# Kernel optimization log

Hardware: AMD Instinct MI355X
Metric: run time of the kernel (lower is better)

The kernel has to match this reference:

```python
import jax, jax.numpy as jnp
import numpy as np

N_LAYER, N_HEAD, D_MODEL, D_K, D_HIDDEN = 8, 8, 512, 64, 2048
N_CONTEXT, N_DICT, MAG = 1024, 8192, 0.05
B, T = 8, 1024


def _sinusoidal_pos(n_context, d_model):
    i2 = np.arange(0, d_model, 2)
    inv = 1.0 / (10000.0 ** (i2 / d_model))
    ang = np.arange(n_context, dtype=np.float32)[:, None] * inv[None, :]
    pe = np.zeros((1, n_context, d_model), np.float32)
    pe[0, :, 0::2] = np.sin(ang)
    pe[0, :, 1::2] = np.cos(ang)
    return jnp.asarray(pe)


def setup_inputs() -> dict:
    key = jax.random.key(0)
    ks = jax.random.split(key, 10)
    p = lambda k, *s: jax.random.normal(k, s, jnp.float32) * MAG
    return {
        "x": jax.random.randint(ks[0], (B, T), 0, N_DICT),
        "last_only": False,
        "capture_stats": False,
        "embedding": p(ks[1], N_DICT, D_MODEL),
        "pos_embedding": _sinusoidal_pos(N_CONTEXT, D_MODEL),  # fixedpos='True', not trained
        "wq": p(ks[2], N_LAYER, N_HEAD, D_MODEL, D_K),
        "wk": p(ks[3], N_LAYER, N_HEAD, D_MODEL, D_K),
        "wv": p(ks[4], N_LAYER, N_HEAD, D_MODEL, D_MODEL),
        "mlp0": p(ks[5], N_LAYER, D_MODEL, D_HIDDEN),
        "mlpb": p(ks[6], N_LAYER, 1, D_HIDDEN),
        "mlp1": p(ks[7], N_LAYER, D_HIDDEN, D_MODEL),
        "unembedding": p(ks[8], D_MODEL, N_DICT),
        "bias": p(ks[9], 1, 1, N_DICT),
    }


def _ln(x):
    # torch LayerNorm(elementwise_affine=False, bias=False), eps=1e-5, biased var
    mu = jnp.mean(x, axis=-1, keepdims=True)
    var = jnp.mean((x - mu) ** 2, axis=-1, keepdims=True)
    return (x - mu) * jax.lax.rsqrt(var + 1e-5)


def reference(x, last_only, capture_stats, embedding, pos_embedding,
              wq, wk, wv, mlp0, mlpb, mlp1, unembedding, bias):
    del capture_stats  # stats path disabled (capture_stats=False)
    t = x.shape[1]
    h = embedding[x] + pos_embedding[:, :t, :]   # [B,T,M]
    h = _ln(h)                                    # enorm='True', lmul = 1/ldiv = 1
    mask = jnp.tril(jnp.ones((t, t), dtype=bool))

    def layer(h, params):
        wq_l, wk_l, wv_l, m0, mb, m1 = params
        q = jnp.einsum('btm,hmq->bhtq', h, wq_l)
        k = jnp.einsum('bom,hmk->bhok', h, wk_l)
        v = jnp.einsum('bom,hmv->bhov', h, wv_l)
        attn = jnp.einsum('bhtq,bhoq->bhto', q, k)
        # exp(clamp(.,max=50)) then tril then sum-normalize (NOT softmax)
        attn = jnp.where(mask, jnp.exp(jnp.minimum(attn, 50.0)), 0.0)
        attn = attn / (jnp.sum(attn, axis=-1, keepdims=True) + 1e-10)
        vsum = jnp.einsum('bhto,bhov->btv', attn, v)  # sums over heads
        h = _ln(h + vsum)                              # amul = 1, lmul = 1
        y = jax.nn.relu(jnp.einsum('btm,mh->bth', h, m0) + mb)
        y = jnp.einsum('bth,hm->btm', y, m1)
        h = _ln(h + y)                                 # pmul = 1, lmul = 1
        return h, None

    h, _ = jax.lax.scan(layer, h, (wq, wk, wv, mlp0, mlpb, mlp1))
    if last_only:
        h = h[:, -1:, :]
    return jnp.einsum('btm,md->btd', h, unembedding) + bias
```

## Files before the change

### kernel.cpp

```cpp
#include <hip/hip_runtime.h>
#include <hip/hip_bf16.h>

#define BB 8
#define TT 1024
#define DM 512
#define NH 8
#define DK 64
#define DH 2048
#define NL 8
#define ND 8192

typedef __attribute__((ext_vector_type(8))) short short8v;
typedef __attribute__((ext_vector_type(8))) _Float16 f16x8;
typedef __attribute__((ext_vector_type(4))) float f32x4;
typedef __attribute__((ext_vector_type(4))) unsigned short ushort4v;
typedef unsigned short u16;

#define MFMA16(a, b, c) __builtin_amdgcn_mfma_f32_16x16x32_bf16(a, b, c, 0, 0, 0)
#define MFMAH(a, b, c)  __builtin_amdgcn_mfma_f32_16x16x32_f16(a, b, c, 0, 0, 0)

__device__ __forceinline__ u16 bf16_bits(float f) {
  union { __hip_bfloat16 h; u16 u; } cv;
  cv.h = __float2bfloat16(f);
  return cv.u;
}
__device__ __forceinline__ float bits_to_f32(u16 u) {
  union { __hip_bfloat16 h; u16 u; } cv;
  cv.u = u;
  return __bfloat162float(cv.h);
}

__device__ __forceinline__ void gload16(const void* g, void* l) {
  __builtin_amdgcn_global_load_lds(
      (const __attribute__((address_space(1))) unsigned int*)g,
      (__attribute__((address_space(3))) unsigned int*)l, 16, 0, 0);
}

#define WAITVM(N) asm volatile("s_waitcnt vmcnt(" #N ")" ::: "memory")
#define BAR() { __builtin_amdgcn_s_barrier(); asm volatile("" ::: "memory"); }

__device__ __forceinline__ void block_reduce2(float& a, float& b) {
  #pragma unroll
  for (int off = 32; off > 0; off >>= 1) {
    a += __shfl_down(a, off, 64);
    b += __shfl_down(b, off, 64);
  }
  __shared__ float sa[4], sb[4];
  int w = threadIdx.x >> 6;
  if ((threadIdx.x & 63) == 0) { sa[w] = a; sb[w] = b; }
  __syncthreads();
  if (threadIdx.x == 0) {
    sa[0] = sa[0] + sa[1] + sa[2] + sa[3];
    sb[0] = sb[0] + sb[1] + sb[2] + sb[3];
  }
  __syncthreads();
  a = sa[0]; b = sb[0];
}

__global__ __launch_bounds__(256) void embed_ln_kernel(
    const int* __restrict__ x, const float* __restrict__ emb,
    const float* __restrict__ pos, float* __restrict__ h,
    u16* __restrict__ hh, _Float16* __restrict__ hf) {
  int bt = blockIdx.x;
  int t = bt & (TT - 1);
  int tid = threadIdx.x;
  int row = x[bt];
  float v0 = emb[(size_t)row * DM + tid]       + pos[(size_t)t * DM + tid];
  float v1 = emb[(size_t)row * DM + tid + 256] + pos[(size_t)t * DM + tid + 256];
  float s = v0 + v1, sq = v0 * v0 + v1 * v1;
  block_reduce2(s, sq);
  float mu  = s * (1.0f / DM);
  float var = sq * (1.0f / DM) - mu * mu;
  float rs  = rsqrtf(var + 1e-5f);
  float r0 = (v0 - mu) * rs, r1 = (v1 - mu) * rs;
  h[(size_t)bt * DM + tid] = r0;
  h[(size_t)bt * DM + tid + 256] = r1;
  hh[(size_t)bt * DM + tid] = bf16_bits(r0);
  hh[(size_t)bt * DM + tid + 256] = bf16_bits(r1);
  hf[(size_t)bt * DM + tid] = (_Float16)r0;
  hf[(size_t)bt * DM + tid + 256] = (_Float16)r1;
}

template<bool BF16ADD>
__global__ __launch_bounds__(256) void ln_residual_kernel(
    float* __restrict__ h, const void* __restrict__ add_, int rowStride, int nsum,
    u16* __restrict__ hh, _Float16* __restrict__ hf) {
  int bt = blockIdx.x;
  int tid = threadIdx.x;
  size_t base = (size_t)bt * (size_t)rowStride;
  float v0 = h[(size_t)bt * DM + tid];
  float v1 = h[(size_t)bt * DM + tid + 256];
  if (BF16ADD) {
    const u16* add = (const u16*)add_;
    for (int i = 0; i < nsum; ++i) {
      v0 += bits_to_f32(add[base + (size_t)i * DM + tid]);
      v1 += bits_to_f32(add[base + (size_t)i * DM + tid + 256]);
    }
  } else {
    const float* add = (const float*)add_;
    for (int i = 0; i < nsum; ++i) {
      v0 += add[base + (size_t)i * DM + tid];
      v1 += add[base + (size_t)i * DM + tid + 256];
    }
  }
  float s = v0 + v1, sq = v0 * v0 + v1 * v1;
  block_reduce2(s, sq);
  float mu  = s * (1.0f / DM);
  float var = sq * (1.0f / DM) - mu * mu;
  float rs  = rsqrtf(var + 1e-5f);
  float r0 = (v0 - mu) * rs, r1 = (v1 - mu) * rs;
  h[(size_t)bt * DM + tid] = r0;
  h[(size_t)bt * DM + tid + 256] = r1;
  hh[(size_t)bt * DM + tid] = bf16_bits(r0);
  hh[(size_t)bt * DM + tid + 256] = bf16_bits(r1);
  hf[(size_t)bt * DM + tid] = (_Float16)r0;
  hf[(size_t)bt * DM + tid + 256] = (_Float16)r1;
}

__global__ __launch_bounds__(256) void transpose_layer(
    const float* __restrict__ wq, const float* __restrict__ wk,
    const float* __restrict__ wv, const float* __restrict__ w0,
    const float* __restrict__ w1,
    _Float16* __restrict__ qT, _Float16* __restrict__ kT,
    u16* __restrict__ vT, u16* __restrict__ t0, u16* __restrict__ t1) {
  __shared__ float T[64][65];
  int t = blockIdx.x;
  const float* in;
  _Float16* of = nullptr;
  u16* ob = nullptr;
  int K, Nb;
  if (t < 64)       { in = wq; of = qT; K = 512;  Nb = 64; }
  else if (t < 128) { in = wk; of = kT; K = 512;  Nb = 64;   t -= 64; }
  else if (t < 640) { in = wv; ob = vT; K = 512;  Nb = 512;  t -= 128; }
  else if (t < 896) { in = w0; ob = t0; K = 512;  Nb = 2048; t -= 640; }
  else              { in = w1; ob = t1; K = 2048; Nb = 512;  t -= 896; }
  int ntx = K >> 6;
  int k0 = (t % ntx) * 64, n0 = (t / ntx) * 64;
  int g = n0 / Nb;
  const float* src = in + (size_t)g * K * Nb + (n0 - g * Nb);
  int tid = threadIdx.x;
  #pragma unroll
  for (int rep = 0; rep < 16; ++rep) {
    int idx = rep * 256 + tid;
    int i = idx >> 6, j = idx & 63;
    T[i][j] = src[(size_t)(k0 + i) * Nb + j];
  }
  __syncthreads();
  #pragma unroll
  for (int rep = 0; rep < 16; ++rep) {
    int idx = rep * 256 + tid;
    int j = idx >> 6, i = idx & 63;
    float v = T[i][j];
    size_t oa = (size_t)(n0 + j) * K + k0 + i;
    if (of) of[oa] = (_Float16)v;
    else    ob[oa] = bf16_bits(v);
  }
}

__global__ __launch_bounds__(256) void transpose_ue(
    const float* __restrict__ ue, u16* __restrict__ ueT) {
  __shared__ float T[64][65];
  int tid = threadIdx.x;
  int k0 = blockIdx.x * 64, n0 = blockIdx.y * 64;
  #pragma unroll
  for (int rep = 0; rep < 16; ++rep) {
    int idx = rep * 256 + tid;
    int i = idx >> 6, j = idx & 63;
    T[i][j] = ue[(size_t)(k0 + i) * ND + n0 + j];
  }
  __syncthreads();
  #pragma unroll
  for (int rep = 0; rep < 16; ++rep) {
    int idx = rep * 256 + tid;
    int j = idx >> 6, i = idx & 63;
    ueT[(size_t)(n0 + j) * DM + k0 + i] = bf16_bits(T[i][j]);
  }
}

template<int MODE>
__global__ __launch_bounds__(256, 2) void gemm_mfma(
    const u16* __restrict__ A, const u16* __restrict__ Bt,
    const float* __restrict__ bias, void* __restrict__ Oo,
    int M, int N, int K) {
  __shared__ u16 As[2][8192];
  __shared__ u16 Bs[2][8192];
  int tid = threadIdx.x;
  int lane = tid & 63, w = tid >> 6;
  int l15 = lane & 15, g = lane >> 4;
  int m0 = blockIdx.x * 128, n0 = blockIdx.y * 128;
  int wr = w >> 1, wc = w & 1;
  int nt = K >> 6;

  f32x4 acc[4][4];
  #pragma unroll
  for (int i = 0; i < 4; ++i)
    #pragma unroll
    for (int j = 0; j < 4; ++j)
      #pragma unroll
      for (int r = 0; r < 4; ++r) acc[i][j][r] = 0.f;

  auto stage = [&](int t, int buf) {
    int k0 = t << 6;
    #pragma unroll
    for (int j = 0; j < 4; ++j) {
      int idx = j * 256 + tid;
      int row = idx >> 3, cs = (idx & 7) ^ (row & 7);
      gload16(A + (size_t)(m0 + row) * K + k0 + cs * 8, &As[buf][idx * 8]);
    }
    #pragma unroll
    for (int j = 0; j < 4; ++j) {
      int idx = j * 256 + tid;
      int row = idx >> 3, cs = (idx & 7) ^ (row & 7);
      gload16(Bt + (size_t)(n0 + row) * K + k0 + cs * 8, &Bs[buf][idx * 8]);
    }
  };

  stage(0, 0);
  for (int t = 0; t < nt; ++t) {
    int cur = t & 1;
    if (t + 1 < nt) {
      stage(t + 1, cur ^ 1);
      WAITVM(8);
    } else {
      WAITVM(0);
    }
    BAR();
    short8v af[4][2], bf[4][2];
    #pragma unroll
    for (int mi = 0; mi < 4; ++mi) {
      int row = wr * 64 + mi * 16 + l15;
      #pragma unroll
      for (int ks = 0; ks < 2; ++ks) {
        int ch = (ks * 4 + g) ^ (row & 7);
        af[mi][ks] = *(const short8v*)&As[cur][row * 64 + ch * 8];
      }
    }
    #pragma unroll
    for (int ni = 0; ni < 4; ++ni) {
      int row = wc * 64 + ni * 16 + l15;
      #pragma unroll
      for (int ks = 0; ks < 2; ++ks) {
        int ch = (ks * 4 + g) ^ (row & 7);
        bf[ni][ks] = *(const short8v*)&Bs[cur][row * 64 + ch * 8];
      }
    }
    __builtin_amdgcn_s_setprio(1);
    #pragma unroll
    for (int mi = 0; mi < 4; ++mi)
      #pragma unroll
      for (int ni = 0; ni < 4; ++ni) {
        acc[mi][ni] = MFMA16(af[mi][0], bf[ni][0], acc[mi][ni]);
        acc[mi][ni] = MFMA16(af[mi][1], bf[ni][1], acc[mi][ni]);
      }
    __builtin_amdgcn_s_setprio(0);
    BAR();
  }

  #pragma unroll
  for (int mi = 0; mi < 4; ++mi) {
    #pragma unroll
    for (int ni = 0; ni < 4; ++ni) {
      int mrow = m0 + wr * 64 + mi * 16 + g * 4;
      int ncol = n0 + wc * 64 + ni * 16 + l15;
      if (MODE == 0) {
        int head = ncol >> 9, dv = ncol & (DM - 1);
        int bb = mrow >> 10, t0 = mrow & (TT - 1);
        ushort4v pk;
        #pragma unroll
        for (int r = 0; r < 4; ++r) pk[r] = bf16_bits(acc[mi][ni][r]);
        *(ushort4v*)((u16*)Oo + ((((size_t)bb * NH + head) * DM + dv) << 10) + t0) = pk;
      } else if (MODE == 1) {
        float bv = bias[ncol];
        #pragma unroll
        for (int r = 0; r < 4; ++r)
          ((u16*)Oo)[(size_t)(mrow + r) * N + ncol] =
              bf16_bits(fmaxf(acc[mi][ni][r] + bv, 0.f));
      } else if (MODE == 2) {
        #pragma unroll
        for (int r = 0; r < 4; ++r)
          ((float*)Oo)[(size_t)(mrow + r) * N + ncol] = acc[mi][ni][r];
      } else {
        float bv = bias[ncol];
        #pragma unroll
        for (int r = 0; r < 4; ++r)
          ((float*)Oo)[(size_t)(mrow + r) * N + ncol] = acc[mi][ni][r] + bv;
      }
    }
  }
}

__global__ __launch_bounds__(256, 2) void gemm_qk_f16(
    const _Float16* __restrict__ A, const _Float16* __restrict__ Bt,
    _Float16* __restrict__ Oq, int K) {
  __shared__ _Float16 As[2][8192];
  __shared__ _Float16 Bs[2][8192];
  int tid = threadIdx.x;
  int lane = tid & 63, w = tid >> 6;
  int l15 = lane & 15, g = lane >> 4;
  int m0 = blockIdx.x * 128, n0 = blockIdx.y * 128;
  int wr = w >> 1, wc = w & 1;
  int nt = K >> 6;

  f32x4 acc[4][4];
  #pragma unroll
  for (int i = 0; i < 4; ++i)
    #pragma unroll
    for (int j = 0; j < 4; ++j)
      #pragma unroll
      for (int r = 0; r < 4; ++r) acc[i][j][r] = 0.f;

  auto stage = [&](int t, int buf) {
    int k0 = t << 6;
    #pragma unroll
    for (int j = 0; j < 4; ++j) {
      int idx = j * 256 + tid;
      int row = idx >> 3, cs = (idx & 7) ^ (row & 7);
      gload16(A + (size_t)(m0 + row) * K + k0 + cs * 8, &As[buf][idx * 8]);
    }
    #pragma unroll
    for (int j = 0; j < 4; ++j) {
      int idx = j * 256 + tid;
      int row = idx >> 3, cs = (idx & 7) ^ (row & 7);
      gload16(Bt + (size_t)(n0 + row) * K + k0 + cs * 8, &Bs[buf][idx * 8]);
    }
  };

  stage(0, 0);
  for (int t = 0; t < nt; ++t) {
    int cur = t & 1;
    if (t + 1 < nt) {
      stage(t + 1, cur ^ 1);
      WAITVM(8);
    } else {
      WAITVM(0);
    }
    BAR();
    f16x8 af[4][2], bf[4][2];
    #pragma unroll
    for (int mi = 0; mi < 4; ++mi) {
      int row = wr * 64 + mi * 16 + l15;
      #pragma unroll
      for (int ks = 0; ks < 2; ++ks) {
        int ch = (ks * 4 + g) ^ (row & 7);
        af[mi][ks] = *(const f16x8*)&As[cur][row * 64 + ch * 8];
      }
    }
    #pragma unroll
    for (int ni = 0; ni < 4; ++ni) {
      int row = wc * 64 + ni * 16 + l15;
      #pragma unroll
      for (int ks = 0; ks < 2; ++ks) {
        int ch = (ks * 4 + g) ^ (row & 7);
        bf[ni][ks] = *(const f16x8*)&Bs[cur][row * 64 + ch * 8];
      }
    }
    __builtin_amdgcn_s_setprio(1);
    #pragma unroll
    for (int mi = 0; mi < 4; ++mi)
      #pragma unroll
      for (int ni = 0; ni < 4; ++ni) {
        acc[mi][ni] = MFMAH(af[mi][0], bf[ni][0], acc[mi][ni]);
        acc[mi][ni] = MFMAH(af[mi][1], bf[ni][1], acc[mi][ni]);
      }
    __builtin_amdgcn_s_setprio(0);
    BAR();
  }

  #pragma unroll
  for (int mi = 0; mi < 4; ++mi) {
    #pragma unroll
    for (int ni = 0; ni < 4; ++ni) {
      int mrow = m0 + wr * 64 + mi * 16 + g * 4;
      int ncol = n0 + wc * 64 + ni * 16 + l15;
      int head = ncol >> 6, dk = ncol & (DK - 1);
      int bb = mrow >> 10;
      #pragma unroll
      for (int r = 0; r < 4; ++r) {
        int t = (mrow + r) & (TT - 1);
        Oq[(((size_t)bb * NH + head) * TT + t) * DK + dk] = (_Float16)acc[mi][ni][r];
      }
    }
  }
}

__global__ __launch_bounds__(256, 2) void attn_mfma_kernel(
    const _Float16* __restrict__ qp, const _Float16* __restrict__ kp,
    const __hip_bfloat16* __restrict__ vt_, u16* __restrict__ o) {
  __shared__ __align__(16) u16 Pl[2][64 * 64];
  __shared__ __align__(16) _Float16 Kl[2][64 * 64];
  __shared__ float rs_lds[64];

  const u16* vtp = (const u16*)vt_;
  int tid = threadIdx.x;
  int lane = tid & 63;
  int w = tid >> 6;
  int l15 = lane & 15, g = lane >> 4;
  int blk = blockIdx.x;
  int bh = blk & 63;
  int tt = 15 - (blk >> 6);

  if (tid < 64) rs_lds[tid] = 0.f;

  auto stageK = [&](int ot, int buf) {
    int ob = ot * 64;
    #pragma unroll
    for (int j = 0; j < 2; ++j) {
      int idx = j * 256 + tid;
      int row = idx >> 3, cs = (idx & 7) ^ (row & 7);
      gload16(kp + ((size_t)bh * TT + ob + row) * DK + cs * 8, &Kl[buf][idx * 8]);
    }
  };

  size_t qbase = (((size_t)bh * TT) + tt * 64 + w * 16 + l15) * DK + g * 8;
  f16x8 qf[2];
  qf[0] = *(const f16x8*)(qp + qbase);
  qf[1] = *(const f16x8*)(qp + qbase + 32);

  f32x4 oacc[4][8];
  #pragma unroll
  for (int qt = 0; qt < 4; ++qt)
    #pragma unroll
    for (int dv = 0; dv < 8; ++dv)
      #pragma unroll
      for (int r = 0; r < 4; ++r) oacc[qt][dv][r] = 0.f;

  stageK(0, 0);
  WAITVM(0);
  __syncthreads();

  for (int ot = 0; ot <= tt; ++ot) {
    int ob = ot * 64;
    bool diag = (ot == tt);
    int buf = ot & 1;
    if (ot < tt) stageK(ot + 1, buf ^ 1);
    f32x4 sacc[4];
    #pragma unroll
    for (int ct = 0; ct < 4; ++ct)
      #pragma unroll
      for (int r = 0; r < 4; ++r) sacc[ct][r] = 0.f;
    __builtin_amdgcn_s_setprio(1);
    #pragma unroll
    for (int ct = 0; ct < 4; ++ct) {
      int row = ct * 16 + l15;
      f16x8 k0 = *(const f16x8*)&Kl[buf][row * 64 + ((g) ^ (row & 7)) * 8];
      f16x8 k1 = *(const f16x8*)&Kl[buf][row * 64 + ((4 + g) ^ (row & 7)) * 8];
      sacc[ct] = MFMAH(qf[0], k0, sacc[ct]);
      sacc[ct] = MFMAH(qf[1], k1, sacc[ct]);
    }
    __builtin_amdgcn_s_setprio(0);
    size_t vbase = ((size_t)bh * DM + w * 128 + l15) * TT + ob + g * 8;
    short8v vf0[8];
    #pragma unroll
    for (int dv = 0; dv < 8; ++dv)
      vf0[dv] = *(const short8v*)(vtp + vbase + (size_t)dv * 16 * TT);
    float psum[4] = {0.f, 0.f, 0.f, 0.f};
    #pragma unroll
    for (int ct = 0; ct < 4; ++ct) {
      #pragma unroll
      for (int r = 0; r < 4; ++r) {
        float s = sacc[ct][r];
        float p = __expf(fminf(s, 50.f));
        if (diag && (ct * 16 + l15 > w * 16 + g * 4 + r)) p = 0.f;
        psum[r] += p;
        int q = w * 16 + g * 4 + r;
        int byte = (q * 128 + (ct * 16 + l15) * 2) ^ ((q & 7) << 4);
        *(u16*)((char*)Pl[buf] + byte) = bf16_bits(p);
      }
    }
    #pragma unroll
    for (int r = 0; r < 4; ++r) {
      float v = psum[r];
      v += __shfl_xor(v, 1, 16);
      v += __shfl_xor(v, 2, 16);
      v += __shfl_xor(v, 4, 16);
      v += __shfl_xor(v, 8, 16);
      if (l15 == 0) rs_lds[w * 16 + g * 4 + r] += v;
    }
    WAITVM(0);
    BAR();
    short8v vf1[8];
    #pragma unroll
    for (int dv = 0; dv < 8; ++dv)
      vf1[dv] = *(const short8v*)(vtp + vbase + 32 + (size_t)dv * 16 * TT);
    short8v pf[4];
    #pragma unroll
    for (int qt = 0; qt < 4; ++qt) {
      int q = qt * 16 + l15;
      int byte = (q * 128 + g * 16) ^ ((q & 7) << 4);
      pf[qt] = *(short8v*)((char*)Pl[buf] + byte);
    }
    __builtin_amdgcn_s_setprio(1);
    #pragma unroll
    for (int dv = 0; dv < 8; ++dv)
      #pragma unroll
      for (int qt = 0; qt < 4; ++qt)
        oacc[qt][dv] = MFMA16(pf[qt], vf0[dv], oacc[qt][dv]);
    __builtin_amdgcn_s_setprio(0);
    #pragma unroll
    for (int qt = 0; qt < 4; ++qt) {
      int q = qt * 16 + l15;
      int byte = (q * 128 + 64 + g * 16) ^ ((q & 7) << 4);
      pf[qt] = *(short8v*)((char*)Pl[buf] + byte);
    }
    __builtin_amdgcn_s_setprio(1);
    #pragma unroll
    for (int dv = 0; dv < 8; ++dv)
      #pragma unroll
      for (int qt = 0; qt < 4; ++qt)
        oacc[qt][dv] = MFMA16(pf[qt], vf1[dv], oacc[qt][dv]);
    __builtin_amdgcn_s_setprio(0);
  }
  __syncthreads();
  int b = bh >> 3, hh2 = bh & 7;
  #pragma unroll
  for (int qt = 0; qt < 4; ++qt) {
    #pragma unroll
    for (int r = 0; r < 4; ++r) {
      int q = qt * 16 + g * 4 + r;
      float rs = 1.0f / (rs_lds[q] + 1e-10f);
      size_t rowbase = ((size_t)(b * TT + tt * 64 + q)) * (NH * DM) + hh2 * DM + w * 128 + l15;
      #pragma unroll
      for (int dv = 0; dv < 8; ++dv)
        o[rowbase + dv * 16] = bf16_bits(oacc[qt][dv][r] * rs);
    }
  }
}

extern "C" void kernel_launch(void* const* d_in, const int* in_sizes, int n_in,
                              void* d_out, int out_size, void* d_ws, size_t ws_size,
                              hipStream_t stream) {
  (void)in_sizes; (void)n_in; (void)out_size; (void)ws_size;
  const int*   x   = (const int*)d_in[0];
  const float* emb = (const float*)d_in[3];
  const float* pos = (const float*)d_in[4];
  const float* wq  = (const float*)d_in[5];
  const float* wk  = (const float*)d_in[6];
  const float* wv  = (const float*)d_in[7];
  const float* m0  = (const float*)d_in[8];
  const float* mb  = (const float*)d_in[9];
  const float* m1  = (const float*)d_in[10];
  const float* ue  = (const float*)d_in[11];
  const float* ub  = (const float*)d_in[12];
  float* out = (float*)d_out;
  float* ws  = (float*)d_ws;

  const int M = BB * TT;

  float*    h    = ws;
  u16*      hh   = (u16*)(ws + 4194304);
  _Float16* hf16 = (_Float16*)(ws + 6291456);
  float*    yb   = ws + 8388608;
  u16*      ueT  = (u16*)(ws + 12582912);

  u16* outus = (u16*)d_out;
  u16* vt = outus;
  _Float16* qf16 = (_Float16*)(outus + 33554432);
  _Float16* kf16 = (_Float16*)(outus + 37748736);
  u16* wT = outus + 41943040;
  _Float16* wqT = (_Float16*)wT;
  _Float16* wkT = (_Float16*)(wT + 262144);
  u16* wvT = wT + 524288;
  u16* w0T = wT + 2621440;
  u16* w1T = wT + 3670016;
  u16* Ob  = outus + 67108864;
  u16* hid = outus;

  embed_ln_kernel<<<M, 256, 0, stream>>>(x, emb, pos, h, hh, hf16);

  for (int l = 0; l < NL; ++l) {
    transpose_layer<<<1152, 256, 0, stream>>>(
        wq + (size_t)l * NH * DM * DK, wk + (size_t)l * NH * DM * DK,
        wv + (size_t)l * NH * DM * DM, m0 + (size_t)l * DM * DH,
        m1 + (size_t)l * DH * DM,
        wqT, wkT, wvT, w0T, w1T);
    gemm_qk_f16<<<dim3(64, 4), 256, 0, stream>>>(hf16, wqT, qf16, DM);
    gemm_qk_f16<<<dim3(64, 4), 256, 0, stream>>>(hf16, wkT, kf16, DM);
    gemm_mfma<0><<<dim3(64, 32), 256, 0, stream>>>(hh, wvT, nullptr, vt, M, NH * DM, DM);
    attn_mfma_kernel<<<BB * NH * (TT / 64), 256, 0, stream>>>(
        qf16, kf16, (const __hip_bfloat16*)vt, Ob);
    ln_residual_kernel<true><<<M, 256, 0, stream>>>(h, Ob, NH * DM, NH, hh, hf16);
    gemm_mfma<1><<<dim3(64, 16), 256, 0, stream>>>(hh, w0T, mb + (size_t)l * DH, hid, M, DH, DM);
    gemm_mfma<2><<<dim3(64, 4), 256, 0, stream>>>(hid, w1T, nullptr, yb, M, DM, DH);
    ln_residual_kernel<false><<<M, 256, 0, stream>>>(h, yb, DM, 1, hh, hf16);
  }
  transpose_ue<<<dim3(8, 128), 256, 0, stream>>>(ue, ueT);
  gemm_mfma<3><<<dim3(64, 64), 256, 0, stream>>>(hh, ueT, ub, out, M, ND, DM);
}
```

Baseline: 2.351 ms.

## Reassociate attention-value product to apply Wv after attention over hidden states

Computes attn·h per head (using a transposed bf16 copy of h) and then multiplies the concatenated head outputs by a stacked Wv (K=4096) in one GEMM. This replaces the large V projection producing 8 heads × 512 dims and the 8-way head summation in the residual LN. The Q and K projections are also merged into a single launch. It adds a per-layer transpose of h and reorders the rounding points, since the attention now runs on bf16 h instead of a bf16 V.

```diff
diff --git a/kernel.cpp b/kernel.cpp
--- a/kernel.cpp
+++ b/kernel.cpp
@@ -83,25 +83,20 @@
 
 template<bool BF16ADD>
 __global__ __launch_bounds__(256) void ln_residual_kernel(
-    float* __restrict__ h, const void* __restrict__ add_, int rowStride, int nsum,
+    float* __restrict__ h, const void* __restrict__ add_,
     u16* __restrict__ hh, _Float16* __restrict__ hf) {
   int bt = blockIdx.x;
   int tid = threadIdx.x;
-  size_t base = (size_t)bt * (size_t)rowStride;
   float v0 = h[(size_t)bt * DM + tid];
   float v1 = h[(size_t)bt * DM + tid + 256];
   if (BF16ADD) {
     const u16* add = (const u16*)add_;
-    for (int i = 0; i < nsum; ++i) {
-      v0 += bits_to_f32(add[base + (size_t)i * DM + tid]);
-      v1 += bits_to_f32(add[base + (size_t)i * DM + tid + 256]);
-    }
+    v0 += bits_to_f32(add[(size_t)bt * DM + tid]);
+    v1 += bits_to_f32(add[(size_t)bt * DM + tid + 256]);
   } else {
     const float* add = (const float*)add_;
-    for (int i = 0; i < nsum; ++i) {
-      v0 += add[base + (size_t)i * DM + tid];
-      v1 += add[base + (size_t)i * DM + tid + 256];
-    }
+    v0 += add[(size_t)bt * DM + tid];
+    v1 += add[(size_t)bt * DM + tid + 256];
   }
   float s = v0 + v1, sq = v0 * v0 + v1 * v1;
   block_reduce2(s, sq);
@@ -117,23 +112,45 @@
   hf[(size_t)bt * DM + tid + 256] = (_Float16)r1;
 }
 
+__global__ __launch_bounds__(256) void transpose_hT(
+    const float* __restrict__ h, u16* __restrict__ hT) {
+  __shared__ float T[64][65];
+  int t0 = blockIdx.x * 64;
+  int d0 = blockIdx.y * 64;
+  int tid = threadIdx.x;
+  #pragma unroll
+  for (int rep = 0; rep < 16; ++rep) {
+    int idx = rep * 256 + tid;
+    int i = idx >> 6, j = idx & 63;
+    T[i][j] = h[(size_t)(t0 + i) * DM + d0 + j];
+  }
+  __syncthreads();
+  #pragma unroll
+  for (int rep = 0; rep < 16; ++rep) {
+    int idx = rep * 256 + tid;
+    int j = idx >> 6, i = idx & 63;
+    hT[(size_t)(d0 + j) * (BB * TT) + t0 + i] = bf16_bits(T[i][j]);
+  }
+}
+
 __global__ __launch_bounds__(256) void transpose_layer(
     const float* __restrict__ wq, const float* __restrict__ wk,
     const float* __restrict__ wv, const float* __restrict__ w0,
     const float* __restrict__ w1,
-    _Float16* __restrict__ qT, _Float16* __restrict__ kT,
-    u16* __restrict__ vT, u16* __restrict__ t0, u16* __restrict__ t1) {
+    _Float16* __restrict__ qkT, u16* __restrict__ vT2,
+    u16* __restrict__ t0o, u16* __restrict__ t1o) {
   __shared__ float T[64][65];
   int t = blockIdx.x;
   const float* in;
   _Float16* of = nullptr;
   u16* ob = nullptr;
   int K, Nb;
-  if (t < 64)       { in = wq; of = qT; K = 512;  Nb = 64; }
-  else if (t < 128) { in = wk; of = kT; K = 512;  Nb = 64;   t -= 64; }
-  else if (t < 640) { in = wv; ob = vT; K = 512;  Nb = 512;  t -= 128; }
-  else if (t < 896) { in = w0; ob = t0; K = 512;  Nb = 2048; t -= 640; }
-  else              { in = w1; ob = t1; K = 2048; Nb = 512;  t -= 896; }
+  bool vmode = false;
+  if (t < 64)       { in = wq; of = qkT;          K = 512;  Nb = 64; }
+  else if (t < 128) { in = wk; of = qkT + 262144; K = 512;  Nb = 64;   t -= 64; }
+  else if (t < 640) { in = wv; ob = vT2;          K = 512;  Nb = 512;  t -= 128; vmode = true; }
+  else if (t < 896) { in = w0; ob = t0o;          K = 512;  Nb = 2048; t -= 640; }
+  else              { in = w1; ob = t1o;          K = 2048; Nb = 512;  t -= 896; }
   int ntx = K >> 6;
   int k0 = (t % ntx) * 64, n0 = (t / ntx) * 64;
   int g = n0 / Nb;
@@ -151,9 +168,13 @@
     int idx = rep * 256 + tid;
     int j = idx >> 6, i = idx & 63;
     float v = T[i][j];
-    size_t oa = (size_t)(n0 + j) * K + k0 + i;
-    if (of) of[oa] = (_Float16)v;
-    else    ob[oa] = bf16_bits(v);
+    if (vmode) {
+      vT2[(size_t)(n0 - g * Nb + j) * (NH * DM) + g * Nb + k0 + i] = bf16_bits(v);
+    } else if (of) {
+      of[(size_t)(n0 + j) * K + k0 + i] = (_Float16)v;
+    } else {
+      ob[(size_t)(n0 + j) * K + k0 + i] = bf16_bits(v);
+    }
   }
 }
 
@@ -262,14 +283,7 @@
     for (int ni = 0; ni < 4; ++ni) {
       int mrow = m0 + wr * 64 + mi * 16 + g * 4;
       int ncol = n0 + wc * 64 + ni * 16 + l15;
-      if (MODE == 0) {
-        int head = ncol >> 9, dv = ncol & (DM - 1);
-        int bb = mrow >> 10, t0 = mrow & (TT - 1);
-        ushort4v pk;
-        #pragma unroll
-        for (int r = 0; r < 4; ++r) pk[r] = bf16_bits(acc[mi][ni][r]);
-        *(ushort4v*)((u16*)Oo + ((((size_t)bb * NH + head) * DM + dv) << 10) + t0) = pk;
-      } else if (MODE == 1) {
+      if (MODE == 1) {
         float bv = bias[ncol];
         #pragma unroll
         for (int r = 0; r < 4; ++r)
@@ -279,11 +293,15 @@
         #pragma unroll
         for (int r = 0; r < 4; ++r)
           ((float*)Oo)[(size_t)(mrow + r) * N + ncol] = acc[mi][ni][r];
-      } else {
+      } else if (MODE == 3) {
         float bv = bias[ncol];
         #pragma unroll
         for (int r = 0; r < 4; ++r)
           ((float*)Oo)[(size_t)(mrow + r) * N + ncol] = acc[mi][ni][r] + bv;
+      } else {
+        #pragma unroll
+        for (int r = 0; r < 4; ++r)
+          ((u16*)Oo)[(size_t)(mrow + r) * N + ncol] = bf16_bits(acc[mi][ni][r]);
       }
     }
   }
@@ -372,12 +390,15 @@
     for (int ni = 0; ni < 4; ++ni) {
       int mrow = m0 + wr * 64 + mi * 16 + g * 4;
       int ncol = n0 + wc * 64 + ni * 16 + l15;
-      int head = ncol >> 6, dk = ncol & (DK - 1);
+      _Float16* dst = Oq;
+      int nc = ncol;
+      if (nc >= 512) { dst = Oq + 4194304; nc -= 512; }
+      int head = nc >> 6, dk = nc & (DK - 1);
       int bb = mrow >> 10;
       #pragma unroll
       for (int r = 0; r < 4; ++r) {
         int t = (mrow + r) & (TT - 1);
-        Oq[(((size_t)bb * NH + head) * TT + t) * DK + dk] = (_Float16)acc[mi][ni][r];
+        dst[(((size_t)bb * NH + head) * TT + t) * DK + dk] = (_Float16)acc[mi][ni][r];
       }
     }
   }
@@ -385,12 +406,11 @@
 
 __global__ __launch_bounds__(256, 2) void attn_mfma_kernel(
     const _Float16* __restrict__ qp, const _Float16* __restrict__ kp,
-    const __hip_bfloat16* __restrict__ vt_, u16* __restrict__ o) {
+    const u16* __restrict__ hT, u16* __restrict__ o) {
   __shared__ __align__(16) u16 Pl[2][64 * 64];
   __shared__ __align__(16) _Float16 Kl[2][64 * 64];
   __shared__ float rs_lds[64];
 
-  const u16* vtp = (const u16*)vt_;
   int tid = threadIdx.x;
   int lane = tid & 63;
   int w = tid >> 6;
@@ -398,6 +418,7 @@
   int blk = blockIdx.x;
   int bh = blk & 63;
   int tt = 15 - (blk >> 6);
+  int b = bh >> 3;
 
   if (tid < 64) rs_lds[tid] = 0.f;
 
@@ -448,11 +469,11 @@
       sacc[ct] = MFMAH(qf[1], k1, sacc[ct]);
     }
     __builtin_amdgcn_s_setprio(0);
-    size_t vbase = ((size_t)bh * DM + w * 128 + l15) * TT + ob + g * 8;
+    size_t vbase = ((size_t)(w * 128 + l15)) * (BB * TT) + b * TT + ob + g * 8;
     short8v vf0[8];
     #pragma unroll
     for (int dv = 0; dv < 8; ++dv)
-      vf0[dv] = *(const short8v*)(vtp + vbase + (size_t)dv * 16 * TT);
+      vf0[dv] = *(const short8v*)(hT + vbase + (size_t)dv * 16 * (BB * TT));
     float psum[4] = {0.f, 0.f, 0.f, 0.f};
     #pragma unroll
     for (int ct = 0; ct < 4; ++ct) {
@@ -481,7 +502,7 @@
     short8v vf1[8];
     #pragma unroll
     for (int dv = 0; dv < 8; ++dv)
-      vf1[dv] = *(const short8v*)(vtp + vbase + 32 + (size_t)dv * 16 * TT);
+      vf1[dv] = *(const short8v*)(hT + vbase + 32 + (size_t)dv * 16 * (BB * TT));
     short8v pf[4];
     #pragma unroll
     for (int qt = 0; qt < 4; ++qt) {
@@ -511,7 +532,7 @@
     __builtin_amdgcn_s_setprio(0);
   }
   __syncthreads();
-  int b = bh >> 3, hh2 = bh & 7;
+  int hh2 = bh & 7;
   #pragma unroll
   for (int qt = 0; qt < 4; ++qt) {
     #pragma unroll
@@ -553,35 +574,36 @@
   u16*      ueT  = (u16*)(ws + 12582912);
 
   u16* outus = (u16*)d_out;
-  u16* vt = outus;
+  u16* hT   = outus;
+  u16* hid  = outus + 4194304;
+  u16* vsum = outus + 20971520;
   _Float16* qf16 = (_Float16*)(outus + 33554432);
-  _Float16* kf16 = (_Float16*)(outus + 37748736);
   u16* wT = outus + 41943040;
-  _Float16* wqT = (_Float16*)wT;
-  _Float16* wkT = (_Float16*)(wT + 262144);
-  u16* wvT = wT + 524288;
-  u16* w0T = wT + 2621440;
-  u16* w1T = wT + 3670016;
-  u16* Ob  = outus + 67108864;
-  u16* hid = outus;
+  _Float16* wqkT = (_Float16*)wT;
+  u16* wvT2 = wT + 524288;
+  u16* w0T  = wT + 2621440;
+  u16* w1T  = wT + 3670016;
+  u16* Ob   = outus + 67108864;
 
   embed_ln_kernel<<<M, 256, 0, stream>>>(x, emb, pos, h, hh, hf16);
+  transpose_hT<<<dim3(128, 8), 256, 0, stream>>>(h, hT);
 
   for (int l = 0; l < NL; ++l) {
     transpose_layer<<<1152, 256, 0, stream>>>(
         wq + (size_t)l * NH * DM * DK, wk + (size_t)l * NH * DM * DK,
         wv + (size_t)l * NH * DM * DM, m0 + (size_t)l * DM * DH,
         m1 + (size_t)l * DH * DM,
-        wqT, wkT, wvT, w0T, w1T);
-    gemm_qk_f16<<<dim3(64, 4), 256, 0, stream>>>(hf16, wqT, qf16, DM);
-    gemm_qk_f16<<<dim3(64, 4), 256, 0, stream>>>(hf16, wkT, kf16, DM);
-    gemm_mfma<0><<<dim3(64, 32), 256, 0, stream>>>(hh, wvT, nullptr, vt, M, NH * DM, DM);
+        wqkT, wvT2, w0T, w1T);
+    gemm_qk_f16<<<dim3(64, 8), 256, 0, stream>>>(hf16, wqkT, qf16, DM);
     attn_mfma_kernel<<<BB * NH * (TT / 64), 256, 0, stream>>>(
-        qf16, kf16, (const __hip_bfloat16*)vt, Ob);
-    ln_residual_kernel<true><<<M, 256, 0, stream>>>(h, Ob, NH * DM, NH, hh, hf16);
+        qf16, qf16 + 4194304, hT, Ob);
+    gemm_mfma<4><<<dim3(64, 4), 256, 0, stream>>>(Ob, wvT2, nullptr, vsum, M, DM, NH * DM);
+    ln_residual_kernel<true><<<M, 256, 0, stream>>>(h, vsum, hh, hf16);
     gemm_mfma<1><<<dim3(64, 16), 256, 0, stream>>>(hh, w0T, mb + (size_t)l * DH, hid, M, DH, DM);
     gemm_mfma<2><<<dim3(64, 4), 256, 0, stream>>>(hid, w1T, nullptr, yb, M, DM, DH);
-    ln_residual_kernel<false><<<M, 256, 0, stream>>>(h, yb, DM, 1, hh, hf16);
+    ln_residual_kernel<false><<<M, 256, 0, stream>>>(h, yb, hh, hf16);
+    if (l + 1 < NL)
+      transpose_hT<<<dim3(128, 8), 256, 0, stream>>>(h, hT);
   }
   transpose_ue<<<dim3(8, 128), 256, 0, stream>>>(ue, ueT);
   gemm_mfma<3><<<dim3(64, 64), 256, 0, stream>>>(hh, ueT, ub, out, M, ND, DM);
```

New measurement: 2.355 ms. About the same (+0.2%).
